# Kernel tuning notes

Measured on AMD Instinct MI355X. Metric: run time of the kernel, lower is better.

Reference implementation:

```python
import jax, jax.numpy as jnp
import numpy as np

N_MET = 200000
N_RXN = 400000
E_SUB = 800000
E_ALL = 1600000
HIDDEN = 64
MSG = 8
DT = 0.01
FRAME = 100
PERIOD = 1000.0
CIRC_AMP = 0.5
HOMEO = 0.1
BASELINE = 1.0


def setup_inputs() -> dict:
    key = jax.random.key(0)
    ks = jax.random.split(key, 12)
    x = jax.random.uniform(ks[0], (N_MET, 8), dtype=jnp.float32)
    met_sub = jax.random.randint(ks[1], (E_SUB,), 0, N_MET, dtype=jnp.int32)
    rxn_sub = jax.random.randint(ks[2], (E_SUB,), 0, N_RXN, dtype=jnp.int32)
    sto_sub = jax.random.uniform(ks[3], (E_SUB,), dtype=jnp.float32, minval=0.5, maxval=2.0)
    met_all = jax.random.randint(ks[4], (E_ALL,), 0, N_MET, dtype=jnp.int32)
    rxn_all = jax.random.randint(ks[5], (E_ALL,), 0, N_RXN, dtype=jnp.int32)
    sto_all = jax.random.normal(ks[6], (E_ALL,), dtype=jnp.float32)
    sub_w1 = jax.random.normal(ks[7], (2, HIDDEN), dtype=jnp.float32) / np.sqrt(2.0)
    sub_b1 = jnp.zeros((HIDDEN,), jnp.float32)
    sub_w2 = jax.random.normal(ks[8], (HIDDEN, MSG), dtype=jnp.float32) / np.sqrt(HIDDEN)
    sub_b2 = jnp.zeros((MSG,), jnp.float32)
    rate_w1 = jax.random.normal(ks[9], (MSG, HIDDEN), dtype=jnp.float32) / np.sqrt(MSG)
    rate_b1 = jnp.zeros((HIDDEN,), jnp.float32)
    rate_w2 = jax.random.normal(ks[10], (HIDDEN, 1), dtype=jnp.float32) / np.sqrt(HIDDEN)
    rate_b2 = jnp.zeros((1,), jnp.float32)
    log_k = jax.random.uniform(ks[11], (N_RXN,), dtype=jnp.float32, minval=-3.0, maxval=-1.0)
    return {"x": x, "met_sub": met_sub, "rxn_sub": rxn_sub, "sto_sub": sto_sub,
            "met_all": met_all, "rxn_all": rxn_all, "sto_all": sto_all,
            "sub_w1": sub_w1, "sub_b1": sub_b1, "sub_w2": sub_w2, "sub_b2": sub_b2,
            "rate_w1": rate_w1, "rate_b1": rate_b1, "rate_w2": rate_w2, "rate_b2": rate_b2,
            "log_k": log_k}


def reference(x, met_sub, rxn_sub, sto_sub, met_all, rxn_all, sto_all,
              sub_w1, sub_b1, sub_w2, sub_b2,
              rate_w1, rate_b1, rate_w2, rate_b2, log_k):
    conc = x[:, 3]                      # [N_MET]
    ext = x[:, 4] * 2.0                 # [N_MET]
    # per-substrate-edge message MLP: [E_SUB,2] -> [E_SUB,MSG]
    msg_in = jnp.stack([conc[met_sub], sto_sub], axis=-1)
    msg = jnp.tanh(msg_in @ sub_w1 + sub_b1) @ sub_w2 + sub_b2
    # scatter-add edge messages into reactions
    h_rxn = jax.ops.segment_sum(msg, rxn_sub, num_segments=N_RXN)  # [N_RXN, MSG]
    k = jnp.power(10.0, log_k)
    base_v = (jnp.tanh(h_rxn @ rate_w1 + rate_b1) @ rate_w2 + rate_b2)[:, 0]  # [N_RXN]
    # multiplicative_substrate modulation: mean external input over substrates
    n_sub = jnp.maximum(
        jax.ops.segment_sum(jnp.ones((E_SUB,), jnp.float32), rxn_sub, num_segments=N_RXN), 1.0)
    ext_mean = jax.ops.segment_sum(ext[met_sub], rxn_sub, num_segments=N_RXN) / n_sub
    v = k * ext_mean * base_v
    # flux limit (dt > 0): no substrate over-consumed in one step
    consumption = sto_sub * v[rxn_sub] * DT
    total = jax.ops.segment_sum(consumption, met_sub, num_segments=N_MET)
    active = total > 1e-12
    met_scale = jnp.where(active,
                          jnp.minimum(conc / jnp.where(active, total, 1.0), 1.0),
                          1.0)
    rxn_scale = jnp.minimum(
        jax.ops.segment_min(met_scale[met_sub], rxn_sub, num_segments=N_RXN), 1.0)
    v = v * rxn_scale
    # scatter stoichiometric contributions to metabolites
    contrib = sto_all * v[rxn_all]
    dxdt = jax.ops.segment_sum(contrib, met_all, num_segments=N_MET)
    # homeostatic relaxation with circadian-modulated constant baseline
    phase = 2.0 * np.pi * FRAME / PERIOD
    modulation = 1.0 + CIRC_AMP * np.sin(phase)
    c_target = BASELINE * modulation
    dxdt = dxdt - HOMEO * (conc - c_target)
    return dxdt[:, None]
```

## Files before the change

kernel.cpp:

```cpp
#include <hip/hip_runtime.h>

#define NMET 200000
#define NRXN 400000
#define ESUB 800000
#define EALL 1600000

#define NBB 196
#define EBA 8192
#define EBS 4096

#define NBUCK_M 391
#define NBUCK_R 782
#define MET_MASK 0x3FFFF
#define MCAP 1280

#define C_TARGET 1.29389262614623664f
#define DT_C 0.01f
#define HOMEO_C 0.1f
#define LOG2_10 3.32192809488736235f

__device__ __forceinline__ float fast_tanh(float x) {
    float e = __expf(2.0f * x);
    return 1.0f - 2.0f * __builtin_amdgcn_rcpf(e + 1.0f);
}

__global__ __launch_bounds__(512) void k_xc(
    const float* __restrict__ x, float2* __restrict__ xc)
{
    int m = blockIdx.x * 512 + threadIdx.x;
    if (m >= NMET) return;
    float2 cx;
    cx.x = x[(size_t)m * 8 + 3];
    cx.y = x[(size_t)m * 8 + 4];
    xc[m] = cx;
}

__global__ __launch_bounds__(512) void k_count_all(
    const int* __restrict__ met_all, const int* __restrict__ met_sub,
    const int* __restrict__ rxn_sub,
    int* __restrict__ blockHistA, int* __restrict__ blockHistS,
    int* __restrict__ blockHistR)
{
    __shared__ int hA[NBUCK_M];
    __shared__ int hS[NBUCK_M];
    __shared__ int hR[NBUCK_R];
    int t = threadIdx.x;
    for (int b = t; b < NBUCK_R; b += 512) hR[b] = 0;
    for (int b = t; b < NBUCK_M; b += 512) { hA[b] = 0; hS[b] = 0; }
    __syncthreads();
    int baseA = blockIdx.x * EBA;
    for (int i = t; i < EBA; i += 512) {
        int e = baseA + i;
        if (e < EALL) atomicAdd(&hA[met_all[e] >> 9], 1);
    }
    int baseS = blockIdx.x * EBS;
    for (int i = t; i < EBS; i += 512) {
        int e = baseS + i;
        if (e < ESUB) {
            atomicAdd(&hS[met_sub[e] >> 9], 1);
            atomicAdd(&hR[rxn_sub[e] >> 9], 1);
        }
    }
    __syncthreads();
    for (int b = t; b < NBUCK_M; b += 512) {
        blockHistA[(size_t)b * NBB + blockIdx.x] = hA[b];
        blockHistS[(size_t)b * NBB + blockIdx.x] = hS[b];
    }
    for (int b = t; b < NBUCK_R; b += 512)
        blockHistR[(size_t)b * NBB + blockIdx.x] = hR[b];
}

__global__ __launch_bounds__(256) void k_scan_all(
    int* __restrict__ blockHistA, int* __restrict__ blockHistS,
    int* __restrict__ blockHistR,
    int* __restrict__ btotalA, int* __restrict__ btotalS,
    int* __restrict__ btotalR)
{
    __shared__ int sc[256];
    int bid = blockIdx.x;
    int* row; int* tot;
    if (bid < NBUCK_M) { row = blockHistA + (size_t)bid * NBB; tot = btotalA + bid; }
    else if (bid < 2 * NBUCK_M) { row = blockHistS + (size_t)(bid - NBUCK_M) * NBB; tot = btotalS + (bid - NBUCK_M); }
    else { row = blockHistR + (size_t)(bid - 2 * NBUCK_M) * NBB; tot = btotalR + (bid - 2 * NBUCK_M); }
    int t = threadIdx.x;
    int val = (t < NBB) ? row[t] : 0;
    sc[t] = val;
    __syncthreads();
    for (int off = 1; off < 256; off <<= 1) {
        int add = (t >= off) ? sc[t - off] : 0;
        __syncthreads();
        sc[t] += add;
        __syncthreads();
    }
    if (t < NBB) row[t] = sc[t] - val;
    if (t == 255) *tot = sc[255];
}

__global__ __launch_bounds__(1024) void k_bstart3(
    const int* __restrict__ btotalA, int* __restrict__ startA,
    const int* __restrict__ btotalS, int* __restrict__ startS,
    const int* __restrict__ btotalR, int* __restrict__ startR)
{
    __shared__ int lds[1024];
    const int* tot; int* st; int nb;
    if (blockIdx.x == 0)      { tot = btotalA; st = startA; nb = NBUCK_M; }
    else if (blockIdx.x == 1) { tot = btotalS; st = startS; nb = NBUCK_M; }
    else                      { tot = btotalR; st = startR; nb = NBUCK_R; }
    int t = threadIdx.x;
    int val = (t < nb) ? tot[t] : 0;
    lds[t] = val;
    __syncthreads();
    for (int off = 1; off < 1024; off <<= 1) {
        int add = (t >= off) ? lds[t - off] : 0;
        __syncthreads();
        lds[t] += add;
        __syncthreads();
    }
    if (t < nb) st[t] = lds[t] - val;
    if (t == 1023) st[nb] = lds[1023];
}

__global__ __launch_bounds__(512) void k_rxn_scatter(
    const int* __restrict__ rxn_sub, const int* __restrict__ met_sub,
    const float* __restrict__ sto_sub,
    const int* __restrict__ blockHistR, const int* __restrict__ bucketStartR,
    uint2* __restrict__ recsR)
{
    __shared__ int cnt[NBUCK_R];
    __shared__ int loff[NBUCK_R];
    __shared__ int rnk[NBUCK_R];
    __shared__ int bbase[NBUCK_R];
    __shared__ unsigned short sbuck[EBS];
    __shared__ uint2 stage[EBS];
    __shared__ int sc[512];
    __shared__ int carry_s;
    int t = threadIdx.x;
    for (int b = t; b < NBUCK_R; b += 512) {
        cnt[b] = 0; rnk[b] = 0;
        bbase[b] = bucketStartR[b] + blockHistR[(size_t)b * NBB + blockIdx.x];
    }
    if (t == 0) carry_s = 0;
    __syncthreads();
    int base = blockIdx.x * EBS;
    int nrec = ESUB - base; if (nrec > EBS) nrec = EBS; if (nrec < 0) nrec = 0;

    for (int i = t; i < nrec; i += 512)
        atomicAdd(&cnt[rxn_sub[base + i] >> 9], 1);
    __syncthreads();
    for (int b0 = 0; b0 < NBUCK_R; b0 += 512) {
        int idx = b0 + t;
        int val = (idx < NBUCK_R) ? cnt[idx] : 0;
        sc[t] = val;
        __syncthreads();
        for (int off = 1; off < 512; off <<= 1) {
            int add = (t >= off) ? sc[t - off] : 0;
            __syncthreads();
            sc[t] += add;
            __syncthreads();
        }
        if (idx < NBUCK_R) loff[idx] = carry_s + sc[t] - val;
        __syncthreads();
        if (t == 511) carry_s += sc[511];
        __syncthreads();
    }
    for (int i = t; i < nrec; i += 512) {
        int e = base + i;
        int r = rxn_sub[e];
        int b = r >> 9;
        int pos = loff[b] + atomicAdd(&rnk[b], 1);
        uint2 rec;
        rec.x = (unsigned)(met_sub[e] | ((r & 511) << 18));
        rec.y = __float_as_uint(sto_sub[e]);
        stage[pos] = rec;
        sbuck[pos] = (unsigned short)b;
    }
    __syncthreads();
    for (int j = t; j < nrec; j += 512) {
        int b = sbuck[j];
        recsR[bbase[b] + (j - loff[b])] = stage[j];
    }
}

__global__ __launch_bounds__(256) void k_csr_bucket(
    const uint2* __restrict__ recsR, const int* __restrict__ bucketStartR,
    int* __restrict__ cntG, int* __restrict__ offG, uint2* __restrict__ recsC)
{
    __shared__ int cnt[512];
    __shared__ int loff[512];
    __shared__ int pscan[256];
    __shared__ int rnk[512];
    int t = threadIdx.x;
    cnt[t] = 0; cnt[t + 256] = 0;
    rnk[t] = 0; rnk[t + 256] = 0;
    __syncthreads();

    int b = blockIdx.x;
    int s = bucketStartR[b], epos = bucketStartR[b + 1];
    for (int i = s + t; i < epos; i += 256)
        atomicAdd(&cnt[(recsR[i].x >> 18) & 511], 1);
    __syncthreads();

    int c0 = cnt[2 * t], c1 = cnt[2 * t + 1];
    int ps = c0 + c1;
    pscan[t] = ps;
    __syncthreads();
    for (int off = 1; off < 256; off <<= 1) {
        int add = (t >= off) ? pscan[t - off] : 0;
        __syncthreads();
        pscan[t] += add;
        __syncthreads();
    }
    int excl = pscan[t] - ps;
    loff[2 * t] = excl;
    loff[2 * t + 1] = excl + c0;
    __syncthreads();

    int gb = b << 9;
    for (int j = t; j < 512; j += 256) {
        cntG[gb + j] = cnt[j];
        offG[gb + j] = s + loff[j];
    }

    for (int i = s + t; i < epos; i += 256) {
        uint2 rec = recsR[i];
        int rloc = (rec.x >> 18) & 511;
        int pos = loff[rloc] + atomicAdd(&rnk[rloc], 1);
        recsC[s + pos] = rec;
    }
}

__global__ __launch_bounds__(512) void k_bucket2(
    const uint2* __restrict__ recsC, const int* __restrict__ bucketStartR,
    const int* __restrict__ cntG, const int* __restrict__ offG,
    const float2* __restrict__ xc,
    const float* __restrict__ sub_w1, const float* __restrict__ sub_b1,
    const float* __restrict__ sub_w2, const float* __restrict__ sub_b2,
    const float* __restrict__ rate_w1, const float* __restrict__ rate_b1,
    const float* __restrict__ rate_w2, const float* __restrict__ rate_b2,
    const float* __restrict__ log_k, float* __restrict__ v)
{
    __shared__ float sW1[128];
    __shared__ float sB1[64];
    __shared__ __align__(16) float sW2[512];
    __shared__ __align__(16) float sR1t[512];
    __shared__ float sRB1[64];
    __shared__ float sR2[64];
    __shared__ float sB2[8];
    __shared__ float sRB2;
    __shared__ float msgL[MCAP][9];
    int t = threadIdx.x;
    sW2[t] = sub_w2[t];
    { int j = t >> 3, k = t & 7; sR1t[t] = rate_w1[k * 64 + j]; }
    if (t < 128) sW1[t] = sub_w1[t];
    if (t < 64) { sB1[t] = sub_b1[t]; sRB1[t] = rate_b1[t]; sR2[t] = rate_w2[t]; }
    if (t < 8) sB2[t] = sub_b2[t];
    if (t == 8) sRB2 = rate_b2[0];
    __syncthreads();

    int b = blockIdx.x;
    int s = bucketStartR[b], epos = bucketStartR[b + 1];
    int gr = (b << 9) + t;
    int n = cntG[gr];
    int base = offG[gr];
    float fn = (float)n;
    float h0 = fn * sB2[0], h1 = fn * sB2[1], h2 = fn * sB2[2], h3 = fn * sB2[3];
    float h4 = fn * sB2[4], h5 = fn * sB2[5], h6 = fn * sB2[6], h7 = fn * sB2[7];
    float exs = 0.f;

    for (int cb = s; cb < epos; cb += MCAP) {
        int ce = epos; if (ce > cb + MCAP) ce = cb + MCAP;
        for (int i = cb + t; i < ce; i += 512) {
            uint2 rec = recsC[i];
            int m = rec.x & MET_MASK;
            float st = __uint_as_float(rec.y);
            float2 cx = xc[m];
            float c  = cx.x;
            float ex = cx.y;
            float m0 = 0.f, m1 = 0.f, m2 = 0.f, m3 = 0.f;
            float m4 = 0.f, m5 = 0.f, m6 = 0.f, m7 = 0.f;
            #pragma unroll 8
            for (int j = 0; j < 64; ++j) {
                float z = fmaf(c, sW1[j], fmaf(st, sW1[64 + j], sB1[j]));
                float th = fast_tanh(z);
                float4 wa = *(const float4*)&sW2[j * 8];
                float4 wb = *(const float4*)&sW2[j * 8 + 4];
                m0 = fmaf(th, wa.x, m0); m1 = fmaf(th, wa.y, m1);
                m2 = fmaf(th, wa.z, m2); m3 = fmaf(th, wa.w, m3);
                m4 = fmaf(th, wb.x, m4); m5 = fmaf(th, wb.y, m5);
                m6 = fmaf(th, wb.z, m6); m7 = fmaf(th, wb.w, m7);
            }
            float* row = msgL[i - cb];
            row[0] = m0; row[1] = m1; row[2] = m2; row[3] = m3;
            row[4] = m4; row[5] = m5; row[6] = m6; row[7] = m7;
            row[8] = ex;
        }
        __syncthreads();
        int lo = base;         if (lo < cb) lo = cb;
        int hi = base + n;     if (hi > ce) hi = ce;
        for (int k = lo; k < hi; ++k) {
            float* row = msgL[k - cb];
            h0 += row[0]; h1 += row[1]; h2 += row[2]; h3 += row[3];
            h4 += row[4]; h5 += row[5]; h6 += row[6]; h7 += row[7];
            exs += row[8];
        }
        __syncthreads();
    }

    if (gr < NRXN) {
        float acc = sRB2;
        #pragma unroll 4
        for (int j = 0; j < 64; ++j) {
            float4 wa = *(const float4*)&sR1t[j * 8];
            float4 wb = *(const float4*)&sR1t[j * 8 + 4];
            float z = sRB1[j];
            z = fmaf(h0, wa.x, z); z = fmaf(h1, wa.y, z);
            z = fmaf(h2, wa.z, z); z = fmaf(h3, wa.w, z);
            z = fmaf(h4, wb.x, z); z = fmaf(h5, wb.y, z);
            z = fmaf(h6, wb.z, z); z = fmaf(h7, wb.w, z);
            acc = fmaf(fast_tanh(z), sR2[j], acc);
        }
        float nmax = fmaxf(fn, 1.0f);
        float ext_mean = 2.0f * exs * __builtin_amdgcn_rcpf(nmax);
        float kk = exp2f(log_k[gr] * LOG2_10);
        v[gr] = kk * ext_mean * acc;
    }
}

__global__ __launch_bounds__(512) void k_cons_scatter(
    const int* __restrict__ met_sub, const int* __restrict__ rxn_sub,
    const float* __restrict__ sto_sub, const float* __restrict__ v,
    const int* __restrict__ blockHistS, const int* __restrict__ bucketStartS,
    uint2* __restrict__ recsS)
{
    __shared__ int cnt[NBUCK_M];
    __shared__ int loff[NBUCK_M];
    __shared__ int rnk[NBUCK_M];
    __shared__ int bbase[NBUCK_M];
    __shared__ int sc[512];
    __shared__ uint2 stage[EBS];
    int t = threadIdx.x;
    for (int b = t; b < NBUCK_M; b += 512) {
        cnt[b] = 0; rnk[b] = 0;
        bbase[b] = bucketStartS[b] + blockHistS[(size_t)b * NBB + blockIdx.x];
    }
    __syncthreads();
    int base = blockIdx.x * EBS;
    int nrec = ESUB - base; if (nrec > EBS) nrec = EBS; if (nrec < 0) nrec = 0;

    for (int i = t; i < nrec; i += 512)
        atomicAdd(&cnt[met_sub[base + i] >> 9], 1);
    __syncthreads();
    int cval = (t < NBUCK_M) ? cnt[t] : 0;
    sc[t] = cval;
    __syncthreads();
    for (int off = 1; off < 512; off <<= 1) {
        int add = (t >= off) ? sc[t - off] : 0;
        __syncthreads();
        sc[t] += add;
        __syncthreads();
    }
    if (t < NBUCK_M) loff[t] = sc[t] - cval;
    __syncthreads();
    for (int i = t; i < nrec; i += 512) {
        int e = base + i;
        int m = met_sub[e];
        int b = m >> 9;
        float val = sto_sub[e] * v[rxn_sub[e]] * DT_C;
        int pos = loff[b] + atomicAdd(&rnk[b], 1);
        uint2 rec;
        rec.x = (unsigned)m;
        rec.y = __float_as_uint(val);
        stage[pos] = rec;
    }
    __syncthreads();
    for (int j = t; j < nrec; j += 512) {
        uint2 rec = stage[j];
        int b = (int)(rec.x >> 9);
        recsS[bbase[b] + (j - loff[b])] = rec;
    }
}

__global__ __launch_bounds__(512) void k_baccum_tot(
    const uint2* __restrict__ recsS, const int* __restrict__ bucketStartS,
    const float* __restrict__ x, float* __restrict__ met_scale)
{
    __shared__ float acc[512];
    int b = blockIdx.x;
    int t = threadIdx.x;
    acc[t] = 0.f;
    __syncthreads();
    int s = bucketStartS[b], epos = bucketStartS[b + 1];
    for (int i = s + t; i < epos; i += 512) {
        uint2 rec = recsS[i];
        atomicAdd(&acc[rec.x & 511], __uint_as_float(rec.y));
    }
    __syncthreads();
    int m = (b << 9) + t;
    if (m < NMET) {
        float tot = acc[t];
        float ms = 1.0f;
        if (tot > 1e-12f) ms = fminf(x[(size_t)m * 8 + 3] / tot, 1.0f);
        met_scale[m] = ms;
    }
}

__global__ __launch_bounds__(256) void k_rscale(
    const int* __restrict__ cntG, const int* __restrict__ offG,
    const uint2* __restrict__ recsC, const float* __restrict__ met_scale,
    float* __restrict__ v)
{
    int r = blockIdx.x * 256 + threadIdx.x;
    if (r >= NRXN) return;
    int n = cntG[r];
    int base = offG[r];
    float ms = 1.0f;
    for (int i = 0; i < n; ++i)
        ms = fminf(ms, met_scale[recsC[base + i].x & MET_MASK]);
    v[r] *= ms;
}

__global__ __launch_bounds__(512) void k_bscatter(
    const int* __restrict__ met_all, const int* __restrict__ rxn_all,
    const float* __restrict__ sto_all, const float* __restrict__ v,
    const int* __restrict__ blockHistA, const int* __restrict__ bucketStartA,
    uint2* __restrict__ recsA)
{
    __shared__ int cnt[NBUCK_M];
    __shared__ int loff[NBUCK_M];
    __shared__ int rnk[NBUCK_M];
    __shared__ int bbase[NBUCK_M];
    __shared__ int sc[512];
    __shared__ uint2 stage[EBA];
    int t = threadIdx.x;
    for (int b = t; b < NBUCK_M; b += 512) {
        cnt[b] = 0; rnk[b] = 0;
        bbase[b] = bucketStartA[b] + blockHistA[(size_t)b * NBB + blockIdx.x];
    }
    __syncthreads();
    int base = blockIdx.x * EBA;
    int nrec = EALL - base; if (nrec > EBA) nrec = EBA; if (nrec < 0) nrec = 0;

    for (int i = t; i < nrec; i += 512)
        atomicAdd(&cnt[met_all[base + i] >> 9], 1);
    __syncthreads();
    int cval = (t < NBUCK_M) ? cnt[t] : 0;
    sc[t] = cval;
    __syncthreads();
    for (int off = 1; off < 512; off <<= 1) {
        int add = (t >= off) ? sc[t - off] : 0;
        __syncthreads();
        sc[t] += add;
        __syncthreads();
    }
    if (t < NBUCK_M) loff[t] = sc[t] - cval;
    __syncthreads();
    for (int i = t; i < nrec; i += 512) {
        int e = base + i;
        int m = met_all[e];
        int b = m >> 9;
        float val = sto_all[e] * v[rxn_all[e]];
        int pos = loff[b] + atomicAdd(&rnk[b], 1);
        uint2 rec;
        rec.x = (unsigned)m;
        rec.y = __float_as_uint(val);
        stage[pos] = rec;
    }
    __syncthreads();
    for (int j = t; j < nrec; j += 512) {
        uint2 rec = stage[j];
        int b = (int)(rec.x >> 9);
        recsA[bbase[b] + (j - loff[b])] = rec;
    }
}

__global__ __launch_bounds__(512) void k_baccum(
    const uint2* __restrict__ recsA, const int* __restrict__ bucketStartA,
    const float* __restrict__ x, float* __restrict__ out)
{
    __shared__ float acc[512];
    int b = blockIdx.x;
    int t = threadIdx.x;
    acc[t] = 0.f;
    __syncthreads();
    int s = bucketStartA[b], epos = bucketStartA[b + 1];
    for (int i = s + t; i < epos; i += 512) {
        uint2 rec = recsA[i];
        atomicAdd(&acc[rec.x & 511], __uint_as_float(rec.y));
    }
    __syncthreads();
    int m = (b << 9) + t;
    if (m < NMET) {
        float c = x[(size_t)m * 8 + 3];
        out[m] = acc[t] - HOMEO_C * (c - C_TARGET);
    }
}

extern "C" void kernel_launch(void* const* d_in, const int* in_sizes, int n_in,
                              void* d_out, int out_size, void* d_ws, size_t ws_size,
                              hipStream_t stream) {
    const float* x       = (const float*)d_in[0];
    const int*   met_sub = (const int*)  d_in[1];
    const int*   rxn_sub = (const int*)  d_in[2];
    const float* sto_sub = (const float*)d_in[3];
    const int*   met_all = (const int*)  d_in[4];
    const int*   rxn_all = (const int*)  d_in[5];
    const float* sto_all = (const float*)d_in[6];
    const float* sub_w1  = (const float*)d_in[7];
    const float* sub_b1  = (const float*)d_in[8];
    const float* sub_w2  = (const float*)d_in[9];
    const float* sub_b2  = (const float*)d_in[10];
    const float* rate_w1 = (const float*)d_in[11];
    const float* rate_b1 = (const float*)d_in[12];
    const float* rate_w2 = (const float*)d_in[13];
    const float* rate_b2 = (const float*)d_in[14];
    const float* log_k   = (const float*)d_in[15];

    char* ws = (char*)d_ws;
    uint2*  recsR = (uint2*)ws;
    uint2*  recsC = recsR + ESUB;
    uint2*  recsS = recsC + ESUB;
    uint2*  recsA = recsS + ESUB;
    float2* xc    = (float2*)(recsA + EALL);
    float*  v     = (float*)(xc + NMET);
    float*  met_scale = v + NRXN;
    int* cntG = (int*)(met_scale + NMET);
    int* offG = cntG + (size_t)NBUCK_R * 512;
    int* blockHistA = offG + (size_t)NBUCK_R * 512;
    int* blockHistS = blockHistA + (size_t)NBUCK_M * NBB;
    int* blockHistR = blockHistS + (size_t)NBUCK_M * NBB;
    int* btotalA = blockHistR + (size_t)NBUCK_R * NBB;
    int* bucketStartA = btotalA + NBUCK_M;
    int* btotalS = bucketStartA + NBUCK_M + 1;
    int* bucketStartS = btotalS + NBUCK_M;
    int* btotalR = bucketStartS + NBUCK_M + 1;
    int* bucketStartR = btotalR + NBUCK_R;
    float* out = (float*)d_out;

    dim3 blk256(256);
    dim3 blk512(512);
    k_xc<<<dim3((NMET + 511) / 512), blk512, 0, stream>>>(x, xc);
    k_count_all<<<dim3(NBB), blk512, 0, stream>>>(
        met_all, met_sub, rxn_sub, blockHistA, blockHistS, blockHistR);
    k_scan_all<<<dim3(2 * NBUCK_M + NBUCK_R), blk256, 0, stream>>>(
        blockHistA, blockHistS, blockHistR, btotalA, btotalS, btotalR);
    k_bstart3<<<dim3(3), dim3(1024), 0, stream>>>(
        btotalA, bucketStartA, btotalS, bucketStartS, btotalR, bucketStartR);
    k_rxn_scatter<<<dim3(NBB), blk512, 0, stream>>>(
        rxn_sub, met_sub, sto_sub, blockHistR, bucketStartR, recsR);
    k_csr_bucket<<<dim3(NBUCK_R), blk256, 0, stream>>>(
        recsR, bucketStartR, cntG, offG, recsC);
    k_bucket2<<<dim3(NBUCK_R), blk512, 0, stream>>>(
        recsC, bucketStartR, cntG, offG, xc,
        sub_w1, sub_b1, sub_w2, sub_b2,
        rate_w1, rate_b1, rate_w2, rate_b2, log_k, v);
    k_cons_scatter<<<dim3(NBB), blk512, 0, stream>>>(
        met_sub, rxn_sub, sto_sub, v, blockHistS, bucketStartS, recsS);
    k_baccum_tot<<<dim3(NBUCK_M), blk512, 0, stream>>>(
        recsS, bucketStartS, x, met_scale);
    k_rscale<<<dim3((NRXN + 255) / 256), blk256, 0, stream>>>(
        cntG, offG, recsC, met_scale, v);
    k_bscatter<<<dim3(NBB), blk512, 0, stream>>>(
        met_all, rxn_all, sto_all, v, blockHistA, bucketStartA, recsA);
    k_baccum<<<dim3(NBUCK_M), blk512, 0, stream>>>(recsA, bucketStartA, x, out);
}
```

Before: 166.7 us.

## Fuse per-reaction CSR bucketing into the message MLP kernel and prescale tanh weights

Removes the separate k_csr_bucket pass. k_bucket2 now counts and scans reactions within each bucket itself, and writes each edge message straight into its sorted slot in shared memory. Only a compact metabolite-index array (metC) is emitted for the later rscale step, replacing the full recsC record array. This drops one kernel launch and a global read/write of the sorted records, and removes the chunked accumulation loop. The catch is that every bucket must now fit in MCAP=1216 shared rows with no overflow check. Separately, the 2*log2(e) factor is folded into the MLP weights so tanh uses exp2 directly, saving a multiply per activation.

```diff
diff --git a/kernel.cpp b/kernel.cpp
--- a/kernel.cpp
+++ b/kernel.cpp
@@ -12,15 +12,20 @@
 #define NBUCK_M 391
 #define NBUCK_R 782
 #define MET_MASK 0x3FFFF
-#define MCAP 1280
+#define MCAP 1216
 
 #define C_TARGET 1.29389262614623664f
 #define DT_C 0.01f
 #define HOMEO_C 0.1f
 #define LOG2_10 3.32192809488736235f
+#define TWO_LOG2E 2.88539008177792677f
 
 __device__ __forceinline__ float fast_tanh(float x) {
     float e = __expf(2.0f * x);
+    return 1.0f - 2.0f * __builtin_amdgcn_rcpf(e + 1.0f);
+}
+__device__ __forceinline__ float tanh_p(float zp) {
+    float e = exp2f(zp);
     return 1.0f - 2.0f * __builtin_amdgcn_rcpf(e + 1.0f);
 }
 
@@ -181,63 +186,15 @@
     }
 }
 
-__global__ __launch_bounds__(256) void k_csr_bucket(
+__global__ __launch_bounds__(512) void k_bucket2(
     const uint2* __restrict__ recsR, const int* __restrict__ bucketStartR,
-    int* __restrict__ cntG, int* __restrict__ offG, uint2* __restrict__ recsC)
-{
-    __shared__ int cnt[512];
-    __shared__ int loff[512];
-    __shared__ int pscan[256];
-    __shared__ int rnk[512];
-    int t = threadIdx.x;
-    cnt[t] = 0; cnt[t + 256] = 0;
-    rnk[t] = 0; rnk[t + 256] = 0;
-    __syncthreads();
-
-    int b = blockIdx.x;
-    int s = bucketStartR[b], epos = bucketStartR[b + 1];
-    for (int i = s + t; i < epos; i += 256)
-        atomicAdd(&cnt[(recsR[i].x >> 18) & 511], 1);
-    __syncthreads();
-
-    int c0 = cnt[2 * t], c1 = cnt[2 * t + 1];
-    int ps = c0 + c1;
-    pscan[t] = ps;
-    __syncthreads();
-    for (int off = 1; off < 256; off <<= 1) {
-        int add = (t >= off) ? pscan[t - off] : 0;
-        __syncthreads();
-        pscan[t] += add;
-        __syncthreads();
-    }
-    int excl = pscan[t] - ps;
-    loff[2 * t] = excl;
-    loff[2 * t + 1] = excl + c0;
-    __syncthreads();
-
-    int gb = b << 9;
-    for (int j = t; j < 512; j += 256) {
-        cntG[gb + j] = cnt[j];
-        offG[gb + j] = s + loff[j];
-    }
-
-    for (int i = s + t; i < epos; i += 256) {
-        uint2 rec = recsR[i];
-        int rloc = (rec.x >> 18) & 511;
-        int pos = loff[rloc] + atomicAdd(&rnk[rloc], 1);
-        recsC[s + pos] = rec;
-    }
-}
-
-__global__ __launch_bounds__(512) void k_bucket2(
-    const uint2* __restrict__ recsC, const int* __restrict__ bucketStartR,
-    const int* __restrict__ cntG, const int* __restrict__ offG,
     const float2* __restrict__ xc,
     const float* __restrict__ sub_w1, const float* __restrict__ sub_b1,
     const float* __restrict__ sub_w2, const float* __restrict__ sub_b2,
     const float* __restrict__ rate_w1, const float* __restrict__ rate_b1,
     const float* __restrict__ rate_w2, const float* __restrict__ rate_b2,
-    const float* __restrict__ log_k, float* __restrict__ v)
+    const float* __restrict__ log_k, float* __restrict__ v,
+    int* __restrict__ cntG, int* __restrict__ offG, int* __restrict__ metC)
 {
     __shared__ float sW1[128];
     __shared__ float sB1[64];
@@ -247,63 +204,86 @@
     __shared__ float sR2[64];
     __shared__ float sB2[8];
     __shared__ float sRB2;
+    __shared__ int cnt[512];
+    __shared__ int loff[512];
     __shared__ float msgL[MCAP][9];
     int t = threadIdx.x;
     sW2[t] = sub_w2[t];
-    { int j = t >> 3, k = t & 7; sR1t[t] = rate_w1[k * 64 + j]; }
-    if (t < 128) sW1[t] = sub_w1[t];
-    if (t < 64) { sB1[t] = sub_b1[t]; sRB1[t] = rate_b1[t]; sR2[t] = rate_w2[t]; }
+    { int j = t >> 3, k = t & 7; sR1t[t] = rate_w1[k * 64 + j] * TWO_LOG2E; }
+    if (t < 128) sW1[t] = sub_w1[t] * TWO_LOG2E;
+    if (t < 64) {
+        sB1[t] = sub_b1[t] * TWO_LOG2E;
+        sRB1[t] = rate_b1[t] * TWO_LOG2E;
+        sR2[t] = rate_w2[t];
+    }
     if (t < 8) sB2[t] = sub_b2[t];
     if (t == 8) sRB2 = rate_b2[0];
+    cnt[t] = 0;
     __syncthreads();
 
     int b = blockIdx.x;
     int s = bucketStartR[b], epos = bucketStartR[b + 1];
     int gr = (b << 9) + t;
-    int n = cntG[gr];
-    int base = offG[gr];
-    float fn = (float)n;
+
+    for (int i = s + t; i < epos; i += 512)
+        atomicAdd(&cnt[(recsR[i].x >> 18) & 511], 1);
+    __syncthreads();
+
+    int val = cnt[t];
+    loff[t] = val;
+    __syncthreads();
+    for (int off = 1; off < 512; off <<= 1) {
+        int add = (t >= off) ? loff[t - off] : 0;
+        __syncthreads();
+        loff[t] += add;
+        __syncthreads();
+    }
+    int excl = loff[t] - val;
+    __syncthreads();
+    loff[t] = excl;
+    cnt[t] = 0;
+    cntG[gr] = val;
+    offG[gr] = s + excl;
+    __syncthreads();
+
+    for (int i = s + t; i < epos; i += 512) {
+        uint2 rec = recsR[i];
+        int m = rec.x & MET_MASK;
+        int rloc = (rec.x >> 18) & 511;
+        float st = __uint_as_float(rec.y);
+        float2 cx = xc[m];
+        float c  = cx.x;
+        float m0 = 0.f, m1 = 0.f, m2 = 0.f, m3 = 0.f;
+        float m4 = 0.f, m5 = 0.f, m6 = 0.f, m7 = 0.f;
+        #pragma unroll 8
+        for (int j = 0; j < 64; ++j) {
+            float zp = fmaf(c, sW1[j], fmaf(st, sW1[64 + j], sB1[j]));
+            float th = tanh_p(zp);
+            float4 wa = *(const float4*)&sW2[j * 8];
+            float4 wb = *(const float4*)&sW2[j * 8 + 4];
+            m0 = fmaf(th, wa.x, m0); m1 = fmaf(th, wa.y, m1);
+            m2 = fmaf(th, wa.z, m2); m3 = fmaf(th, wa.w, m3);
+            m4 = fmaf(th, wb.x, m4); m5 = fmaf(th, wb.y, m5);
+            m6 = fmaf(th, wb.z, m6); m7 = fmaf(th, wb.w, m7);
+        }
+        int pos = loff[rloc] + atomicAdd(&cnt[rloc], 1);
+        float* row = msgL[pos];
+        row[0] = m0; row[1] = m1; row[2] = m2; row[3] = m3;
+        row[4] = m4; row[5] = m5; row[6] = m6; row[7] = m7;
+        row[8] = cx.y;
+        metC[s + pos] = m;
+    }
+    __syncthreads();
+
+    float fn = (float)val;
     float h0 = fn * sB2[0], h1 = fn * sB2[1], h2 = fn * sB2[2], h3 = fn * sB2[3];
     float h4 = fn * sB2[4], h5 = fn * sB2[5], h6 = fn * sB2[6], h7 = fn * sB2[7];
     float exs = 0.f;
-
-    for (int cb = s; cb < epos; cb += MCAP) {
-        int ce = epos; if (ce > cb + MCAP) ce = cb + MCAP;
-        for (int i = cb + t; i < ce; i += 512) {
-            uint2 rec = recsC[i];
-            int m = rec.x & MET_MASK;
-            float st = __uint_as_float(rec.y);
-            float2 cx = xc[m];
-            float c  = cx.x;
-            float ex = cx.y;
-            float m0 = 0.f, m1 = 0.f, m2 = 0.f, m3 = 0.f;
-            float m4 = 0.f, m5 = 0.f, m6 = 0.f, m7 = 0.f;
-            #pragma unroll 8
-            for (int j = 0; j < 64; ++j) {
-                float z = fmaf(c, sW1[j], fmaf(st, sW1[64 + j], sB1[j]));
-                float th = fast_tanh(z);
-                float4 wa = *(const float4*)&sW2[j * 8];
-                float4 wb = *(const float4*)&sW2[j * 8 + 4];
-                m0 = fmaf(th, wa.x, m0); m1 = fmaf(th, wa.y, m1);
-                m2 = fmaf(th, wa.z, m2); m3 = fmaf(th, wa.w, m3);
-                m4 = fmaf(th, wb.x, m4); m5 = fmaf(th, wb.y, m5);
-                m6 = fmaf(th, wb.z, m6); m7 = fmaf(th, wb.w, m7);
-            }
-            float* row = msgL[i - cb];
-            row[0] = m0; row[1] = m1; row[2] = m2; row[3] = m3;
-            row[4] = m4; row[5] = m5; row[6] = m6; row[7] = m7;
-            row[8] = ex;
-        }
-        __syncthreads();
-        int lo = base;         if (lo < cb) lo = cb;
-        int hi = base + n;     if (hi > ce) hi = ce;
-        for (int k = lo; k < hi; ++k) {
-            float* row = msgL[k - cb];
-            h0 += row[0]; h1 += row[1]; h2 += row[2]; h3 += row[3];
-            h4 += row[4]; h5 += row[5]; h6 += row[6]; h7 += row[7];
-            exs += row[8];
-        }
-        __syncthreads();
+    for (int i = 0; i < val; ++i) {
+        float* row = msgL[excl + i];
+        h0 += row[0]; h1 += row[1]; h2 += row[2]; h3 += row[3];
+        h4 += row[4]; h5 += row[5]; h6 += row[6]; h7 += row[7];
+        exs += row[8];
     }
 
     if (gr < NRXN) {
@@ -312,12 +292,12 @@
         for (int j = 0; j < 64; ++j) {
             float4 wa = *(const float4*)&sR1t[j * 8];
             float4 wb = *(const float4*)&sR1t[j * 8 + 4];
-            float z = sRB1[j];
-            z = fmaf(h0, wa.x, z); z = fmaf(h1, wa.y, z);
-            z = fmaf(h2, wa.z, z); z = fmaf(h3, wa.w, z);
-            z = fmaf(h4, wb.x, z); z = fmaf(h5, wb.y, z);
-            z = fmaf(h6, wb.z, z); z = fmaf(h7, wb.w, z);
-            acc = fmaf(fast_tanh(z), sR2[j], acc);
+            float zp = sRB1[j];
+            zp = fmaf(h0, wa.x, zp); zp = fmaf(h1, wa.y, zp);
+            zp = fmaf(h2, wa.z, zp); zp = fmaf(h3, wa.w, zp);
+            zp = fmaf(h4, wb.x, zp); zp = fmaf(h5, wb.y, zp);
+            zp = fmaf(h6, wb.z, zp); zp = fmaf(h7, wb.w, zp);
+            acc = fmaf(tanh_p(zp), sR2[j], acc);
         }
         float nmax = fmaxf(fn, 1.0f);
         float ext_mean = 2.0f * exs * __builtin_amdgcn_rcpf(nmax);
@@ -406,7 +386,7 @@
 
 __global__ __launch_bounds__(256) void k_rscale(
     const int* __restrict__ cntG, const int* __restrict__ offG,
-    const uint2* __restrict__ recsC, const float* __restrict__ met_scale,
+    const int* __restrict__ metC, const float* __restrict__ met_scale,
     float* __restrict__ v)
 {
     int r = blockIdx.x * 256 + threadIdx.x;
@@ -415,7 +395,7 @@
     int base = offG[r];
     float ms = 1.0f;
     for (int i = 0; i < n; ++i)
-        ms = fminf(ms, met_scale[recsC[base + i].x & MET_MASK]);
+        ms = fminf(ms, met_scale[metC[base + i]]);
     v[r] *= ms;
 }
 
@@ -517,11 +497,11 @@
 
     char* ws = (char*)d_ws;
     uint2*  recsR = (uint2*)ws;
-    uint2*  recsC = recsR + ESUB;
-    uint2*  recsS = recsC + ESUB;
+    uint2*  recsS = recsR + ESUB;
     uint2*  recsA = recsS + ESUB;
     float2* xc    = (float2*)(recsA + EALL);
-    float*  v     = (float*)(xc + NMET);
+    int*    metC  = (int*)(xc + NMET);
+    float*  v     = (float*)(metC + ESUB);
     float*  met_scale = v + NRXN;
     int* cntG = (int*)(met_scale + NMET);
     int* offG = cntG + (size_t)NBUCK_R * 512;
@@ -547,18 +527,16 @@
         btotalA, bucketStartA, btotalS, bucketStartS, btotalR, bucketStartR);
     k_rxn_scatter<<<dim3(NBB), blk512, 0, stream>>>(
         rxn_sub, met_sub, sto_sub, blockHistR, bucketStartR, recsR);
-    k_csr_bucket<<<dim3(NBUCK_R), blk256, 0, stream>>>(
-        recsR, bucketStartR, cntG, offG, recsC);
     k_bucket2<<<dim3(NBUCK_R), blk512, 0, stream>>>(
-        recsC, bucketStartR, cntG, offG, xc,
+        recsR, bucketStartR, xc,
         sub_w1, sub_b1, sub_w2, sub_b2,
-        rate_w1, rate_b1, rate_w2, rate_b2, log_k, v);
+        rate_w1, rate_b1, rate_w2, rate_b2, log_k, v, cntG, offG, metC);
     k_cons_scatter<<<dim3(NBB), blk512, 0, stream>>>(
         met_sub, rxn_sub, sto_sub, v, blockHistS, bucketStartS, recsS);
     k_baccum_tot<<<dim3(NBUCK_M), blk512, 0, stream>>>(
         recsS, bucketStartS, x, met_scale);
     k_rscale<<<dim3((NRXN + 255) / 256), blk256, 0, stream>>>(
-        cntG, offG, recsC, met_scale, v);
+        cntG, offG, metC, met_scale, v);
     k_bscatter<<<dim3(NBB), blk512, 0, stream>>>(
         met_all, rxn_all, sto_all, v, blockHistA, bucketStartA, recsA);
     k_baccum<<<dim3(NBUCK_M), blk512, 0, stream>>>(recsA, bucketStartA, x, out);
```

Result: no change. 167.9 us (+0.7%).
